# Optimization experiments

Measured on AMD Instinct MI355X. Metric: run time of the kernel, lower is better.

## Reference

```python
import jax, jax.numpy as jnp
import numpy as np

B, S, EPG = 1024, 64, 256          # graphs, nodes per graph, edges per graph
N, E = B * S, B * EPG              # 65536 nodes, 262144 edges
D, H = 128, 4                      # hidden dim, attention heads
DH = D // H
INIT_DIM, EDGE_DIM = 9, 3
N_EXTRA = 3                        # n_layers - 1
NEG_SLOPE = 0.2


def _gatv2(x, src, dst, edge_attr, Wl, Wr, bl, br, We, att, bias, heads, out_dim, concat):
    # PyG GATv2Conv with edge features: m = leaky_relu(xl[src]+xr[dst]+We@e),
    # alpha = segment_softmax(<m,att>, dst), out = scatter_add(alpha*xl[src], dst)
    n = x.shape[0]
    xl = (x @ Wl + bl).reshape(n, heads, out_dim)
    xr = (x @ Wr + br).reshape(n, heads, out_dim)
    ee = (edge_attr @ We).reshape(-1, heads, out_dim)
    m = jax.nn.leaky_relu(xl[src] + xr[dst] + ee, NEG_SLOPE)      # [E,H,O]
    logit = (m * att[None]).sum(-1)                               # [E,H]
    mx = jax.ops.segment_max(logit, dst, num_segments=n)
    ex = jnp.exp(logit - mx[dst])
    den = jax.ops.segment_sum(ex, dst, num_segments=n)
    alpha = ex / den[dst]                                         # segment softmax over in-edges
    out = jax.ops.segment_sum(xl[src] * alpha[:, :, None], dst, num_segments=n)
    out = out.reshape(n, heads * out_dim) if concat else out.mean(axis=1)
    return out + bias


def _forward(x, edge_index, edge_attr,
             g0_Wl, g0_Wr, g0_bl, g0_br, g0_We, g0_att, g0_bias,
             gWl, gWr, gbl, gbr, gWe, gatt, gbias,
             Wq, Wk, Wv, bq, bk, bv, Wo, bo):
    src, dst = edge_index[0], edge_index[1]
    h = _gatv2(x, src, dst, edge_attr, g0_Wl, g0_Wr, g0_bl, g0_br, g0_We, g0_att, g0_bias, 1, D, True)
    for i in range(N_EXTRA):
        h = (_gatv2(jax.nn.relu(h), src, dst, edge_attr,
                    gWl[i], gWr[i], gbl[i], gbr[i], gWe[i], gatt[i], gbias[i],
                    H, D, False) + h) / 2
    # to_dense_batch: equal-size graphs -> exact reshape, mask all True
    xd = h.reshape(B, S, D)
    q = (xd @ Wq + bq).reshape(B, S, H, DH)
    k = (xd @ Wk + bk).reshape(B, S, H, DH)
    v = (xd @ Wv + bv).reshape(B, S, H, DH)
    att = jax.nn.softmax(jnp.einsum('bqhd,bkhd->bhqk', q, k) / np.float32(np.sqrt(DH)), axis=-1)
    o = jnp.einsum('bhqk,bkhd->bqhd', att, v).reshape(B, S, D) @ Wo + bo
    return (h + o.reshape(N, D)) / 2


def setup_inputs():
    key = jax.random.key(0)
    ks = jax.random.split(key, 16)

    def gl(k, shape, fan):
        return jax.random.normal(k, shape, jnp.float32) / np.float32(np.sqrt(fan))

    x = jax.random.normal(ks[0], (N, INIT_DIM), jnp.float32)
    # random intra-graph edges: local indices in [0,S) offset per graph
    local = jax.random.randint(ks[1], (2, B, EPG), 0, S)
    edge_index = (local + (jnp.arange(B) * S)[None, :, None]).reshape(2, E)
    edge_attr = jax.random.normal(ks[2], (E, EDGE_DIM), jnp.float32)
    batch = jnp.repeat(jnp.arange(B), S)
    return dict(
        x=x, edge_index=edge_index, edge_attr=edge_attr, batch=batch,
        g0_Wl=gl(ks[3], (INIT_DIM, D), INIT_DIM), g0_Wr=gl(ks[4], (INIT_DIM, D), INIT_DIM),
        g0_bl=jnp.zeros((D,), jnp.float32), g0_br=jnp.zeros((D,), jnp.float32),
        g0_We=gl(ks[5], (EDGE_DIM, D), EDGE_DIM), g0_att=gl(ks[6], (1, D), D),
        g0_bias=jnp.zeros((D,), jnp.float32),
        gWl=gl(ks[7], (N_EXTRA, D, H * D), D), gWr=gl(ks[8], (N_EXTRA, D, H * D), D),
        gbl=jnp.zeros((N_EXTRA, H * D), jnp.float32), gbr=jnp.zeros((N_EXTRA, H * D), jnp.float32),
        gWe=gl(ks[9], (N_EXTRA, EDGE_DIM, H * D), EDGE_DIM), gatt=gl(ks[10], (N_EXTRA, H, D), D),
        gbias=jnp.zeros((N_EXTRA, D), jnp.float32),
        Wq=gl(ks[11], (D, D), D), Wk=gl(ks[12], (D, D), D), Wv=gl(ks[13], (D, D), D),
        bq=jnp.zeros((D,), jnp.float32), bk=jnp.zeros((D,), jnp.float32), bv=jnp.zeros((D,), jnp.float32),
        Wo=gl(ks[14], (D, D), D), bo=jnp.zeros((D,), jnp.float32),
    )


def reference(x, edge_index, edge_attr, batch,
              g0_Wl, g0_Wr, g0_bl, g0_br, g0_We, g0_att, g0_bias,
              gWl, gWr, gbl, gbr, gWe, gatt, gbias,
              Wq, Wk, Wv, bq, bk, bv, Wo, bo):
    # batch is implied by the equal-graph layout (reshape in _forward)
    return _forward(x, edge_index, edge_attr,
                    g0_Wl, g0_Wr, g0_bl, g0_br, g0_We, g0_att, g0_bias,
                    gWl, gWr, gbl, gbr, gWe, gatt, gbias,
                    Wq, Wk, Wv, bq, bk, bv, Wo, bo)
```

## Files before the change

kernel.cpp:

```cpp
#include <hip/hip_runtime.h>

constexpr int Bg  = 1024;
constexpr int Sg  = 64;
constexpr int EPG = 256;
constexpr int Nn  = Bg * Sg;
constexpr int Ne  = Bg * EPG;
constexpr int NH  = 4;
constexpr float NEG = 0.2f;

constexpr int CHUNK_G = 512;
constexpr int CHUNK_N = CHUNK_G * Sg;

typedef float  f32x4  __attribute__((ext_vector_type(4)));
typedef short  s16x8  __attribute__((ext_vector_type(8)));
typedef unsigned short u16x4 __attribute__((ext_vector_type(4)));

static __device__ __forceinline__ unsigned fenc(float f) {
    unsigned u = __float_as_uint(f);
    return (u & 0x80000000u) ? ~u : (u | 0x80000000u);
}
static __device__ __forceinline__ float fdec(unsigned k) {
    unsigned u = (k & 0x80000000u) ? (k ^ 0x80000000u) : ~k;
    return __uint_as_float(u);
}
static __device__ __forceinline__ unsigned short bf16rn(float x) {
    unsigned u = __float_as_uint(x);
    u += 0x7FFFu + ((u >> 16) & 1u);
    return (unsigned short)(u >> 16);
}
static __device__ __forceinline__ float bf16f(unsigned short h) {
    return __uint_as_float((unsigned)h << 16);
}
static __device__ __forceinline__ unsigned pack32(float x) {
    unsigned u  = __float_as_uint(x);
    unsigned hb = u & 0xffff0000u;
    float lof   = x - __uint_as_float(hb);
    return hb | (__float_as_uint(lof) >> 16);
}
static __device__ __forceinline__ float up_hi(unsigned u) {
    return __uint_as_float(u & 0xffff0000u);
}
static __device__ __forceinline__ float up_lo(unsigned u) {
    return __uint_as_float(u << 16);
}
#define DPP_ADD(x, ctrl) \
    ((x) + __int_as_float(__builtin_amdgcn_update_dpp( \
        0, __float_as_int(x), (ctrl), 0xF, 0xF, true)))

__global__ __launch_bounds__(256)
void wprep(const float* __restrict__ gWl, const float* __restrict__ gWr,
           const float* __restrict__ Wq, const float* __restrict__ Wk,
           const float* __restrict__ Wv, const float* __restrict__ Wo,
           unsigned short* __restrict__ whi, unsigned short* __restrict__ wlo) {
    int gid = blockIdx.x, t = threadIdx.x;
    const float* src;
    int n, k;
    size_t oidx;
    if (gid < 1536) {
        int s = gid >> 8;
        int e = ((gid & 255) << 8) + t;
        n = e & 511; k = e >> 9;
        src = (s & 1) ? (gWr + (s >> 1) * 65536) : (gWl + (s >> 1) * 65536);
        oidx = (size_t)s * 65536 + n * 128 + k;
        float v = src[k * 512 + n];
        unsigned short h = bf16rn(v);
        whi[oidx] = h;
        wlo[oidx] = bf16rn(v - bf16f(h));
    } else {
        int g2 = gid - 1536;
        int s = g2 >> 6;
        int e = ((g2 & 63) << 8) + t;
        n = e & 127; k = e >> 7;
        src = (s == 0) ? Wq : (s == 1) ? Wk : (s == 2) ? Wv : Wo;
        oidx = 393216 + (size_t)s * 16384 + n * 128 + k;
        float v = src[k * 128 + n];
        unsigned short h = bf16rn(v);
        whi[oidx] = h;
        wlo[oidx] = bf16rn(v - bf16f(h));
    }
}

__global__ __launch_bounds__(256)
void proj0(const float* __restrict__ x, const float* __restrict__ Wl,
           const float* __restrict__ Wr, const float* __restrict__ bl,
           const float* __restrict__ br, float* __restrict__ xl0,
           float* __restrict__ xr0) {
    int t = blockIdx.x * 256 + threadIdx.x;
    int n = t >> 7, j = t & 127;
    float xv[9];
#pragma unroll
    for (int k = 0; k < 9; ++k) xv[k] = x[n * 9 + k];
    float al = bl[j], ar = br[j];
#pragma unroll
    for (int k = 0; k < 9; ++k) {
        al = fmaf(xv[k], Wl[k * 128 + j], al);
        ar = fmaf(xv[k], Wr[k * 128 + j], ar);
    }
    xl0[t] = al;
    xr0[t] = ar;
}

template<bool RELU, int EPI>
__global__ __launch_bounds__(256, 2)
void gemm_mfma(const float* __restrict__ A, const unsigned short* __restrict__ wth,
               const unsigned short* __restrict__ wtl, const float* __restrict__ bias,
               const float* __restrict__ res, float* __restrict__ C, int NC) {
    __shared__ __align__(16) char smem[65536];
    constexpr int AH = 0, AL = 16384, BH = 32768, BL = 49152;

    const int t = threadIdx.x;
    const int r0 = blockIdx.y * 128, c0 = blockIdx.x * 128;
    const int wave = t >> 6, lane = t & 63;
    const int wm = wave >> 1, wn = wave & 1;
    const int lr = lane & 15, lg = lane >> 4;

    f32x4 acc[4][4] = {};

    int rowA[4], rowB[4];
#pragma unroll
    for (int i = 0; i < 4; ++i) {
        rowA[i] = wm * 64 + i * 16 + lr;
        rowB[i] = wn * 64 + i * 16 + lr;
    }

    for (int kc = 0; kc < 2; ++kc) {
#pragma unroll
        for (int i = 0; i < 8; ++i) {
            int f = t + i * 256;
            int row = f >> 4;
            int c4  = (f & 15) << 2;
            float4 v = *reinterpret_cast<const float4*>(
                &A[(size_t)(r0 + row) * 128 + kc * 64 + c4]);
            if (RELU) {
                v.x = fmaxf(v.x, 0.f); v.y = fmaxf(v.y, 0.f);
                v.z = fmaxf(v.z, 0.f); v.w = fmaxf(v.w, 0.f);
            }
            unsigned short h0 = bf16rn(v.x), h1 = bf16rn(v.y),
                           h2 = bf16rn(v.z), h3 = bf16rn(v.w);
            u16x4 hp = {h0, h1, h2, h3};
            u16x4 lp = {bf16rn(v.x - bf16f(h0)), bf16rn(v.y - bf16f(h1)),
                        bf16rn(v.z - bf16f(h2)), bf16rn(v.w - bf16f(h3))};
            int off = row * 128 + ((c4 * 2) ^ ((row & 7) << 4));
            *reinterpret_cast<u16x4*>(smem + AH + off) = hp;
            *reinterpret_cast<u16x4*>(smem + AL + off) = lp;
        }
#pragma unroll
        for (int i = 0; i < 4; ++i) {
            int f = t + i * 256;
            int row = f >> 3;
            int c8  = (f & 7) << 3;
            size_t gsrc = (size_t)(c0 + row) * 128 + kc * 64 + c8;
            s16x8 hv = *reinterpret_cast<const s16x8*>(&wth[gsrc]);
            s16x8 lv = *reinterpret_cast<const s16x8*>(&wtl[gsrc]);
            int off = row * 128 + ((c8 * 2) ^ ((row & 7) << 4));
            *reinterpret_cast<s16x8*>(smem + BH + off) = hv;
            *reinterpret_cast<s16x8*>(smem + BL + off) = lv;
        }
        __syncthreads();

#pragma unroll
        for (int ks = 0; ks < 2; ++ks) {
            const int kb = ks * 64 + lg * 16;
            s16x8 ah[4], al4[4];
#pragma unroll
            for (int mi = 0; mi < 4; ++mi) {
                int off = rowA[mi] * 128 + (kb ^ ((rowA[mi] & 7) << 4));
                ah[mi]  = *reinterpret_cast<const s16x8*>(smem + AH + off);
                al4[mi] = *reinterpret_cast<const s16x8*>(smem + AL + off);
            }
#pragma unroll
            for (int ni = 0; ni < 4; ++ni) {
                int off = rowB[ni] * 128 + (kb ^ ((rowB[ni] & 7) << 4));
                s16x8 bh = *reinterpret_cast<const s16x8*>(smem + BH + off);
                s16x8 bl = *reinterpret_cast<const s16x8*>(smem + BL + off);
#pragma unroll
                for (int mi = 0; mi < 4; ++mi) {
                    acc[mi][ni] = __builtin_amdgcn_mfma_f32_16x16x32_bf16(
                        ah[mi], bh, acc[mi][ni], 0, 0, 0);
                    acc[mi][ni] = __builtin_amdgcn_mfma_f32_16x16x32_bf16(
                        ah[mi], bl, acc[mi][ni], 0, 0, 0);
                    acc[mi][ni] = __builtin_amdgcn_mfma_f32_16x16x32_bf16(
                        al4[mi], bh, acc[mi][ni], 0, 0, 0);
                }
            }
        }
        __syncthreads();
    }

#pragma unroll
    for (int ni = 0; ni < 4; ++ni) {
        int c = c0 + wn * 64 + ni * 16 + lr;
        float bs = bias[c];
#pragma unroll
        for (int mi = 0; mi < 4; ++mi) {
#pragma unroll
            for (int j = 0; j < 4; ++j) {
                int r = r0 + wm * 64 + mi * 16 + lg * 4 + j;
                float ov = acc[mi][ni][j] + bs;
                if (EPI == 1) ov = (ov + res[(size_t)r * 128 + c]) * 0.5f;
                C[(size_t)r * NC + c] = ov;
            }
        }
    }
}

template<int HEADS, int EPI>
__global__ __launch_bounds__(512, 4)
void gat_edge(const float* __restrict__ xl, const float* __restrict__ xr,
              const int* __restrict__ ei, const float* __restrict__ ea,
              const float* __restrict__ We, const float* __restrict__ att,
              const float* __restrict__ bias, const float* __restrict__ hres,
              float* __restrict__ hout, int g0) {
    constexpr int WROW = HEADS * 128;
    __shared__ __align__(16) unsigned xli[64 * 128];
    __shared__ __align__(16) unsigned xri[64 * 128];
    __shared__ float eas[EPG * 4];
    __shared__ float logit[EPG];
    __shared__ int   se[EPG], de[EPG];
    __shared__ unsigned nmax[64];
    __shared__ float nden[64];

    const int g = g0 + blockIdx.x;
    const int t = threadIdx.x, lane = t & 63, wave = t >> 6;
    const int lr = lane & 15, lg = lane >> 4;
    const int wm = wave >> 2, wn = wave & 3;

    if (t < EPG) {
        se[t] = ei[g * EPG + t] - g * 64;
        de[t] = ei[Ne + g * EPG + t] - g * 64;
        eas[t * 4 + 0] = ea[(size_t)(g * EPG + t) * 3 + 0];
        eas[t * 4 + 1] = ea[(size_t)(g * EPG + t) * 3 + 1];
        eas[t * 4 + 2] = ea[(size_t)(g * EPG + t) * 3 + 2];
    }

    f32x4 acc[2][2] = {};
    float* P32 = reinterpret_cast<float*>(xri);

    for (int hh = 0; hh < HEADS; ++hh) {
        __syncthreads();
#pragma unroll
        for (int i = 0; i < 4; ++i) {
            int f  = t + i * 512;
            int r  = f >> 5;
            int c4 = (f & 31) << 2;
            size_t nl = (size_t)((g - g0) * 64 + r);
            float4 vl = *reinterpret_cast<const float4*>(&xl[nl * WROW + hh * 128 + c4]);
            float4 vr = *reinterpret_cast<const float4*>(&xr[nl * WROW + hh * 128 + c4]);
            uint4 pl = {pack32(vl.x), pack32(vl.y), pack32(vl.z), pack32(vl.w)};
            uint4 pr = {pack32(vr.x), pack32(vr.y), pack32(vr.z), pack32(vr.w)};
            *reinterpret_cast<uint4*>(&xli[r * 128 + c4]) = pl;
            *reinterpret_cast<uint4*>(&xri[r * 128 + c4]) = pr;
        }
        if (t < 64) { nmax[t] = 0u; nden[t] = 0.f; }
        __syncthreads();

        const float a1 = att[hh * 128 + 2 * lane];
        const float a2 = att[hh * 128 + 2 * lane + 1];
        float we1[3], we2[3];
#pragma unroll
        for (int k = 0; k < 3; ++k) {
            we1[k] = We[k * WROW + hh * 128 + 2 * lane];
            we2[k] = We[k * WROW + hh * 128 + 2 * lane + 1];
        }

        for (int e = wave; e < EPG; e += 8) {
            int s_ = se[e], d_ = de[e];
            float4 ev = *reinterpret_cast<const float4*>(&eas[e * 4]);
            uint2 ul = *reinterpret_cast<const uint2*>(&xli[s_ * 128 + 2 * lane]);
            uint2 ur = *reinterpret_cast<const uint2*>(&xri[d_ * 128 + 2 * lane]);
            float m1 = up_hi(ul.x) + up_lo(ul.x) + up_hi(ur.x) + up_lo(ur.x)
                       + ev.x * we1[0] + ev.y * we1[1] + ev.z * we1[2];
            float m2 = up_hi(ul.y) + up_lo(ul.y) + up_hi(ur.y) + up_lo(ur.y)
                       + ev.x * we2[0] + ev.y * we2[1] + ev.z * we2[2];
            m1 = m1 > 0.f ? m1 : NEG * m1;
            m2 = m2 > 0.f ? m2 : NEG * m2;
            float r = fmaf(m1, a1, m2 * a2);
            r = DPP_ADD(r, 0x111);
            r = DPP_ADD(r, 0x112);
            r = DPP_ADD(r, 0x114);
            r = DPP_ADD(r, 0x118);
            r = DPP_ADD(r, 0x142);
            r = DPP_ADD(r, 0x143);
            if (lane == 63) logit[e] = r;
        }
        __syncthreads();

        for (int i = t; i < 1088; i += 512)
            reinterpret_cast<float4*>(P32)[i] = float4{0.f, 0.f, 0.f, 0.f};
        if (t < EPG) atomicMax(&nmax[de[t]], fenc(logit[t]));
        __syncthreads();
        float ex = 0.f;
        if (t < EPG) {
            ex = __expf(logit[t] - fdec(nmax[de[t]]));
            atomicAdd(&nden[de[t]], ex);
        }
        __syncthreads();
        if (t < EPG) atomicAdd(&P32[de[t] * 68 + se[t]], ex / nden[de[t]]);
        __syncthreads();

#pragma unroll
        for (int ks = 0; ks < 2; ++ks) {
            s16x8 bh[2], bl[2];
#pragma unroll
            for (int nt = 0; nt < 2; ++nt) {
                int n = wn * 32 + nt * 16 + lr;
                unsigned uu[8];
#pragma unroll
                for (int j = 0; j < 8; ++j)
                    uu[j] = xli[(ks * 32 + lg * 8 + j) * 128 + n];
#pragma unroll
                for (int j = 0; j < 8; ++j) {
                    bh[nt][j] = (short)(uu[j] >> 16);
                    bl[nt][j] = (short)(uu[j] & 0xffffu);
                }
            }
#pragma unroll
            for (int mi = 0; mi < 2; ++mi) {
                const float* pr = &P32[(wm * 32 + mi * 16 + lr) * 68 + ks * 32 + lg * 8];
                float4 p0 = *reinterpret_cast<const float4*>(pr);
                float4 p1 = *reinterpret_cast<const float4*>(pr + 4);
                float pv[8] = {p0.x, p0.y, p0.z, p0.w, p1.x, p1.y, p1.z, p1.w};
                s16x8 pah, pal;
#pragma unroll
                for (int j = 0; j < 8; ++j) {
                    unsigned u = __float_as_uint(pv[j]);
                    unsigned hb = u & 0xffff0000u;
                    pah[j] = (short)(u >> 16);
                    pal[j] = (short)(__float_as_uint(pv[j] - __uint_as_float(hb)) >> 16);
                }
#pragma unroll
                for (int nt = 0; nt < 2; ++nt) {
                    acc[mi][nt] = __builtin_amdgcn_mfma_f32_16x16x32_bf16(
                        pah, bh[nt], acc[mi][nt], 0, 0, 0);
                    acc[mi][nt] = __builtin_amdgcn_mfma_f32_16x16x32_bf16(
                        pah, bl[nt], acc[mi][nt], 0, 0, 0);
                    acc[mi][nt] = __builtin_amdgcn_mfma_f32_16x16x32_bf16(
                        pal, bh[nt], acc[mi][nt], 0, 0, 0);
                }
            }
        }
    }

    constexpr float inv = 1.0f / (float)HEADS;
#pragma unroll
    for (int mi = 0; mi < 2; ++mi) {
#pragma unroll
        for (int nt = 0; nt < 2; ++nt) {
            int c_ = wn * 32 + nt * 16 + lr;
            float bs = bias[c_];
#pragma unroll
            for (int j = 0; j < 4; ++j) {
                int r_ = wm * 32 + mi * 16 + lg * 4 + j;
                size_t gi = (size_t)(g * 64 + r_) * 128 + c_;
                float v = acc[mi][nt][j] * inv + bs;
                if (EPI == 1) v = (v + hres[gi]) * 0.5f;
                hout[gi] = v;
            }
        }
    }
}

__global__ __launch_bounds__(256, 3)
void attn_k(const float* __restrict__ q, const float* __restrict__ k,
            const float* __restrict__ v, float* __restrict__ o) {
    __shared__ __align__(16) float qT[32 * 68];
    __shared__ __align__(16) float kT[32 * 68];
    __shared__ __align__(16) float vs[64 * 36];
    __shared__ __align__(16) float St[64 * 68];
    __shared__ float rden[64];

    const int g = blockIdx.x >> 2, hh = blockIdx.x & 3;
    const int t = threadIdx.x;

#pragma unroll
    for (int i = 0; i < 2; ++i) {
        int f = t + i * 256;
        int row = f >> 3;
        int c4  = (f & 7) << 2;
        size_t gi = (size_t)(g * 64 + row) * 128 + hh * 32 + c4;
        float4 qv = *reinterpret_cast<const float4*>(&q[gi]);
        float4 kv = *reinterpret_cast<const float4*>(&k[gi]);
        float4 vv = *reinterpret_cast<const float4*>(&v[gi]);
        qT[(c4 + 0) * 68 + row] = qv.x; qT[(c4 + 1) * 68 + row] = qv.y;
        qT[(c4 + 2) * 68 + row] = qv.z; qT[(c4 + 3) * 68 + row] = qv.w;
        kT[(c4 + 0) * 68 + row] = kv.x; kT[(c4 + 1) * 68 + row] = kv.y;
        kT[(c4 + 2) * 68 + row] = kv.z; kT[(c4 + 3) * 68 + row] = kv.w;
        *reinterpret_cast<float4*>(&vs[row * 36 + c4]) = vv;
    }
    __syncthreads();

    {
        const int rg = (t & 15) << 2, cg = (t >> 4) << 2;
        float acc[4][4] = {};
#pragma unroll 8
        for (int kk = 0; kk < 32; ++kk) {
            float4 qv = *reinterpret_cast<const float4*>(&qT[kk * 68 + rg]);
            float4 kv = *reinterpret_cast<const float4*>(&kT[kk * 68 + cg]);
            acc[0][0] = fmaf(qv.x, kv.x, acc[0][0]);
            acc[0][1] = fmaf(qv.x, kv.y, acc[0][1]);
            acc[0][2] = fmaf(qv.x, kv.z, acc[0][2]);
            acc[0][3] = fmaf(qv.x, kv.w, acc[0][3]);
            acc[1][0] = fmaf(qv.y, kv.x, acc[1][0]);
            acc[1][1] = fmaf(qv.y, kv.y, acc[1][1]);
            acc[1][2] = fmaf(qv.y, kv.z, acc[1][2]);
            acc[1][3] = fmaf(qv.y, kv.w, acc[1][3]);
            acc[2][0] = fmaf(qv.z, kv.x, acc[2][0]);
            acc[2][1] = fmaf(qv.z, kv.y, acc[2][1]);
            acc[2][2] = fmaf(qv.z, kv.z, acc[2][2]);
            acc[2][3] = fmaf(qv.z, kv.w, acc[2][3]);
            acc[3][0] = fmaf(qv.w, kv.x, acc[3][0]);
            acc[3][1] = fmaf(qv.w, kv.y, acc[3][1]);
            acc[3][2] = fmaf(qv.w, kv.z, acc[3][2]);
            acc[3][3] = fmaf(qv.w, kv.w, acc[3][3]);
        }
        constexpr float sc = 0.17677669529663687f;
#pragma unroll
        for (int j = 0; j < 4; ++j) {
            float4 sv;
            sv.x = acc[0][j] * sc; sv.y = acc[1][j] * sc;
            sv.z = acc[2][j] * sc; sv.w = acc[3][j] * sc;
            *reinterpret_cast<float4*>(&St[(cg + j) * 68 + rg]) = sv;
        }
    }
    __syncthreads();

    {
        const int r = t >> 2, q4 = t & 3;
        float mx = -3.4e38f;
#pragma unroll
        for (int i = 0; i < 16; ++i)
            mx = fmaxf(mx, St[(q4 * 16 + i) * 68 + r]);
        mx = fmaxf(mx, __shfl_xor(mx, 1, 64));
        mx = fmaxf(mx, __shfl_xor(mx, 2, 64));
        float sm = 0.f;
#pragma unroll
        for (int i = 0; i < 16; ++i) {
            int idx = (q4 * 16 + i) * 68 + r;
            float e = __expf(St[idx] - mx);
            St[idx] = e;
            sm += e;
        }
        sm += __shfl_xor(sm, 1, 64);
        sm += __shfl_xor(sm, 2, 64);
        if (q4 == 0) rden[r] = 1.f / sm;
    }
    __syncthreads();

    {
        const int rg = (t & 15) << 2, dg = (t >> 4) << 1;
        float a0 = 0.f, a1 = 0.f, a2 = 0.f, a3 = 0.f;
        float b0 = 0.f, b1 = 0.f, b2 = 0.f, b3 = 0.f;
#pragma unroll 8
        for (int kk = 0; kk < 64; ++kk) {
            float4 pv = *reinterpret_cast<const float4*>(&St[kk * 68 + rg]);
            float2 vv = *reinterpret_cast<const float2*>(&vs[kk * 36 + dg]);
            a0 = fmaf(pv.x, vv.x, a0); b0 = fmaf(pv.x, vv.y, b0);
            a1 = fmaf(pv.y, vv.x, a1); b1 = fmaf(pv.y, vv.y, b1);
            a2 = fmaf(pv.z, vv.x, a2); b2 = fmaf(pv.z, vv.y, b2);
            a3 = fmaf(pv.w, vv.x, a3); b3 = fmaf(pv.w, vv.y, b3);
        }
        float4 rd = *reinterpret_cast<const float4*>(&rden[rg]);
        float2 o0 = {a0 * rd.x, b0 * rd.x};
        float2 o1 = {a1 * rd.y, b1 * rd.y};
        float2 o2 = {a2 * rd.z, b2 * rd.z};
        float2 o3 = {a3 * rd.w, b3 * rd.w};
        size_t gb = (size_t)(g * 64 + rg) * 128 + hh * 32 + dg;
        *reinterpret_cast<float2*>(&o[gb])       = o0;
        *reinterpret_cast<float2*>(&o[gb + 128]) = o1;
        *reinterpret_cast<float2*>(&o[gb + 256]) = o2;
        *reinterpret_cast<float2*>(&o[gb + 384]) = o3;
    }
}

extern "C" void kernel_launch(void* const* d_in, const int* in_sizes, int n_in,
                              void* d_out, int out_size, void* d_ws, size_t ws_size,
                              hipStream_t stream) {
    const float* x     = (const float*)d_in[0];
    const int*   ei    = (const int*)d_in[1];
    const float* ea    = (const float*)d_in[2];
    const float* g0Wl  = (const float*)d_in[4];
    const float* g0Wr  = (const float*)d_in[5];
    const float* g0bl  = (const float*)d_in[6];
    const float* g0br  = (const float*)d_in[7];
    const float* g0We  = (const float*)d_in[8];
    const float* g0att = (const float*)d_in[9];
    const float* g0bias= (const float*)d_in[10];
    const float* gWl   = (const float*)d_in[11];
    const float* gWr   = (const float*)d_in[12];
    const float* gbl   = (const float*)d_in[13];
    const float* gbr   = (const float*)d_in[14];
    const float* gWe   = (const float*)d_in[15];
    const float* gatt  = (const float*)d_in[16];
    const float* gbias = (const float*)d_in[17];
    const float* Wq    = (const float*)d_in[18];
    const float* Wk    = (const float*)d_in[19];
    const float* Wv    = (const float*)d_in[20];
    const float* bq    = (const float*)d_in[21];
    const float* bk    = (const float*)d_in[22];
    const float* bv    = (const float*)d_in[23];
    const float* Wo    = (const float*)d_in[24];
    const float* bo    = (const float*)d_in[25];
    float* out = (float*)d_out;
    float* ws  = (float*)d_ws;

    float* h   = ws;
    float* xlb = ws + (size_t)Nn * 128;
    float* xrb = xlb + (size_t)CHUNK_N * 512;
    float* qb = xlb;
    float* kb = xlb + (size_t)Nn * 128;
    float* vb = xrb;
    float* ob = xrb + (size_t)Nn * 128;
    unsigned short* whi = (unsigned short*)(xrb + (size_t)CHUNK_N * 512);
    unsigned short* wlo = whi + 458752;

    wprep<<<1792, 256, 0, stream>>>(gWl, gWr, Wq, Wk, Wv, Wo, whi, wlo);

    proj0<<<Nn * 128 / 256, 256, 0, stream>>>(x, g0Wl, g0Wr, g0bl, g0br, xlb, xrb);
    gat_edge<1, 0><<<Bg, 512, 0, stream>>>(xlb, xrb, ei, ea, g0We, g0att,
                                           g0bias, nullptr, h, 0);

    for (int i = 0; i < 3; ++i) {
        for (int c = 0; c < 2; ++c) {
            const float* Ain = h + (size_t)c * CHUNK_N * 128;
            dim3 grid(512 / 128, CHUNK_N / 128);
            gemm_mfma<true, 0><<<grid, 256, 0, stream>>>(
                Ain, whi + (size_t)(2 * i) * 65536, wlo + (size_t)(2 * i) * 65536,
                gbl + i * 512, nullptr, xlb, 512);
            gemm_mfma<true, 0><<<grid, 256, 0, stream>>>(
                Ain, whi + (size_t)(2 * i + 1) * 65536, wlo + (size_t)(2 * i + 1) * 65536,
                gbr + i * 512, nullptr, xrb, 512);
            gat_edge<4, 1><<<CHUNK_G, 512, 0, stream>>>(
                xlb, xrb, ei, ea, gWe + (size_t)i * 3 * 512,
                gatt + (size_t)i * 4 * 128, gbias + i * 128, h, h, c * CHUNK_G);
        }
    }

    {
        dim3 grid(1, Nn / 128);
        gemm_mfma<false, 0><<<grid, 256, 0, stream>>>(h, whi + 393216, wlo + 393216,
                                                      bq, nullptr, qb, 128);
        gemm_mfma<false, 0><<<grid, 256, 0, stream>>>(h, whi + 409600, wlo + 409600,
                                                      bk, nullptr, kb, 128);
        gemm_mfma<false, 0><<<grid, 256, 0, stream>>>(h, whi + 425984, wlo + 425984,
                                                      bv, nullptr, vb, 128);
        attn_k<<<Bg * NH, 256, 0, stream>>>(qb, kb, vb, ob);
        gemm_mfma<false, 1><<<grid, 256, 0, stream>>>(ob, whi + 442368, wlo + 442368,
                                                      bo, h, out, 128);
    }
}
```

Before: 1.049 ms.

## Store intermediates in packed bf16 hi/lo format and swizzle GAT shared memory

Changes the storage format of xl/xr and h between kernels to packed 32-bit bf16 hi/lo pairs. Producers (proj0, gemm epilogue, gat_edge) write packed values and consumers split them directly, with no per-load fp32→bf16 conversion. ReLU on packed values becomes a sign-bit check. It also adds an XOR swizzle to the gat_edge shared-memory node tiles to reduce bank conflicts in the edge gather and MFMA B-operand reads. Memory traffic is unchanged (still 32 bits per element); the saving is in conversion ALU work and LDS conflicts. Precision changes slightly, because the final residual now uses the reconstructed hi+lo sum of h instead of the full fp32 value.

Measured after the change: 1.075 ms. 1.02x slower.

```diff
diff --git a/kernel.cpp b/kernel.cpp
--- a/kernel.cpp
+++ b/kernel.cpp
@@ -43,6 +43,13 @@
 static __device__ __forceinline__ float up_lo(unsigned u) {
     return __uint_as_float(u << 16);
 }
+static __device__ __forceinline__ float unpk(unsigned u) {
+    return up_hi(u) + up_lo(u);
+}
+static __device__ __forceinline__ unsigned relu_pk(unsigned u) {
+    return ((int)u < 0) ? 0u : u;
+}
+#define SWZ(r) (((((r) >> 3) & 1) << 4) | ((((r) >> 3) & 2) << 1))
 #define DPP_ADD(x, ctrl) \
     ((x) + __int_as_float(__builtin_amdgcn_update_dpp( \
         0, __float_as_int(x), (ctrl), 0xF, 0xF, true)))
@@ -83,8 +90,8 @@
 __global__ __launch_bounds__(256)
 void proj0(const float* __restrict__ x, const float* __restrict__ Wl,
            const float* __restrict__ Wr, const float* __restrict__ bl,
-           const float* __restrict__ br, float* __restrict__ xl0,
-           float* __restrict__ xr0) {
+           const float* __restrict__ br, unsigned* __restrict__ xl0,
+           unsigned* __restrict__ xr0) {
     int t = blockIdx.x * 256 + threadIdx.x;
     int n = t >> 7, j = t & 127;
     float xv[9];
@@ -96,15 +103,15 @@
         al = fmaf(xv[k], Wl[k * 128 + j], al);
         ar = fmaf(xv[k], Wr[k * 128 + j], ar);
     }
-    xl0[t] = al;
-    xr0[t] = ar;
-}
-
-template<bool RELU, int EPI>
+    xl0[t] = pack32(al);
+    xr0[t] = pack32(ar);
+}
+
+template<int IN_MODE, int OUT_MODE>
 __global__ __launch_bounds__(256, 2)
-void gemm_mfma(const float* __restrict__ A, const unsigned short* __restrict__ wth,
+void gemm_mfma(const void* __restrict__ Av, const unsigned short* __restrict__ wth,
                const unsigned short* __restrict__ wtl, const float* __restrict__ bias,
-               const float* __restrict__ res, float* __restrict__ C, int NC) {
+               const unsigned* __restrict__ hres, void* __restrict__ Cv, int NC) {
     __shared__ __align__(16) char smem[65536];
     constexpr int AH = 0, AL = 16384, BH = 32768, BL = 49152;
 
@@ -129,17 +136,27 @@
             int f = t + i * 256;
             int row = f >> 4;
             int c4  = (f & 15) << 2;
-            float4 v = *reinterpret_cast<const float4*>(
-                &A[(size_t)(r0 + row) * 128 + kc * 64 + c4]);
-            if (RELU) {
-                v.x = fmaxf(v.x, 0.f); v.y = fmaxf(v.y, 0.f);
-                v.z = fmaxf(v.z, 0.f); v.w = fmaxf(v.w, 0.f);
-            }
-            unsigned short h0 = bf16rn(v.x), h1 = bf16rn(v.y),
-                           h2 = bf16rn(v.z), h3 = bf16rn(v.w);
-            u16x4 hp = {h0, h1, h2, h3};
-            u16x4 lp = {bf16rn(v.x - bf16f(h0)), bf16rn(v.y - bf16f(h1)),
-                        bf16rn(v.z - bf16f(h2)), bf16rn(v.w - bf16f(h3))};
+            u16x4 hp, lp;
+            if (IN_MODE == 0) {
+                float4 v = *reinterpret_cast<const float4*>(
+                    &((const float*)Av)[(size_t)(r0 + row) * 128 + kc * 64 + c4]);
+                unsigned short h0 = bf16rn(v.x), h1 = bf16rn(v.y),
+                               h2 = bf16rn(v.z), h3 = bf16rn(v.w);
+                hp = u16x4{h0, h1, h2, h3};
+                lp = u16x4{bf16rn(v.x - bf16f(h0)), bf16rn(v.y - bf16f(h1)),
+                           bf16rn(v.z - bf16f(h2)), bf16rn(v.w - bf16f(h3))};
+            } else {
+                uint4 u = *reinterpret_cast<const uint4*>(
+                    &((const unsigned*)Av)[(size_t)(r0 + row) * 128 + kc * 64 + c4]);
+                if (IN_MODE == 2) {
+                    u.x = relu_pk(u.x); u.y = relu_pk(u.y);
+                    u.z = relu_pk(u.z); u.w = relu_pk(u.w);
+                }
+                hp = u16x4{(unsigned short)(u.x >> 16), (unsigned short)(u.y >> 16),
+                           (unsigned short)(u.z >> 16), (unsigned short)(u.w >> 16)};
+                lp = u16x4{(unsigned short)(u.x & 0xffffu), (unsigned short)(u.y & 0xffffu),
+                           (unsigned short)(u.z & 0xffffu), (unsigned short)(u.w & 0xffffu)};
+            }
             int off = row * 128 + ((c4 * 2) ^ ((row & 7) << 4));
             *reinterpret_cast<u16x4*>(smem + AH + off) = hp;
             *reinterpret_cast<u16x4*>(smem + AL + off) = lp;
@@ -197,8 +214,14 @@
             for (int j = 0; j < 4; ++j) {
                 int r = r0 + wm * 64 + mi * 16 + lg * 4 + j;
                 float ov = acc[mi][ni][j] + bs;
-                if (EPI == 1) ov = (ov + res[(size_t)r * 128 + c]) * 0.5f;
-                C[(size_t)r * NC + c] = ov;
+                if (OUT_MODE == 0) {
+                    ((unsigned*)Cv)[(size_t)r * NC + c] = pack32(ov);
+                } else if (OUT_MODE == 1) {
+                    ((float*)Cv)[(size_t)r * NC + c] = ov;
+                } else {
+                    ov = (ov + unpk(hres[(size_t)r * 128 + c])) * 0.5f;
+                    ((float*)Cv)[(size_t)r * NC + c] = ov;
+                }
             }
         }
     }
@@ -206,11 +229,11 @@
 
 template<int HEADS, int EPI>
 __global__ __launch_bounds__(512, 4)
-void gat_edge(const float* __restrict__ xl, const float* __restrict__ xr,
+void gat_edge(const unsigned* __restrict__ xl, const unsigned* __restrict__ xr,
               const int* __restrict__ ei, const float* __restrict__ ea,
               const float* __restrict__ We, const float* __restrict__ att,
-              const float* __restrict__ bias, const float* __restrict__ hres,
-              float* __restrict__ hout, int g0) {
+              const float* __restrict__ bias, const unsigned* __restrict__ hres,
+              unsigned* __restrict__ hout, int g0) {
     constexpr int WROW = HEADS * 128;
     __shared__ __align__(16) unsigned xli[64 * 128];
     __shared__ __align__(16) unsigned xri[64 * 128];
@@ -224,6 +247,7 @@
     const int t = threadIdx.x, lane = t & 63, wave = t >> 6;
     const int lr = lane & 15, lg = lane >> 4;
     const int wm = wave >> 2, wn = wave & 3;
+    const int swzB = ((lg & 1) << 4) | ((lg & 2) << 1);
 
     if (t < EPG) {
         se[t] = ei[g * EPG + t] - g * 64;
@@ -244,12 +268,11 @@
             int r  = f >> 5;
             int c4 = (f & 31) << 2;
             size_t nl = (size_t)((g - g0) * 64 + r);
-            float4 vl = *reinterpret_cast<const float4*>(&xl[nl * WROW + hh * 128 + c4]);
-            float4 vr = *reinterpret_cast<const float4*>(&xr[nl * WROW + hh * 128 + c4]);
-            uint4 pl = {pack32(vl.x), pack32(vl.y), pack32(vl.z), pack32(vl.w)};
-            uint4 pr = {pack32(vr.x), pack32(vr.y), pack32(vr.z), pack32(vr.w)};
-            *reinterpret_cast<uint4*>(&xli[r * 128 + c4]) = pl;
-            *reinterpret_cast<uint4*>(&xri[r * 128 + c4]) = pr;
+            uint4 pl = *reinterpret_cast<const uint4*>(&xl[nl * WROW + hh * 128 + c4]);
+            uint4 pr = *reinterpret_cast<const uint4*>(&xr[nl * WROW + hh * 128 + c4]);
+            int cs = c4 ^ SWZ(r);
+            *reinterpret_cast<uint4*>(&xli[r * 128 + cs]) = pl;
+            *reinterpret_cast<uint4*>(&xri[r * 128 + cs]) = pr;
         }
         if (t < 64) { nmax[t] = 0u; nden[t] = 0.f; }
         __syncthreads();
@@ -266,11 +289,13 @@
         for (int e = wave; e < EPG; e += 8) {
             int s_ = se[e], d_ = de[e];
             float4 ev = *reinterpret_cast<const float4*>(&eas[e * 4]);
-            uint2 ul = *reinterpret_cast<const uint2*>(&xli[s_ * 128 + 2 * lane]);
-            uint2 ur = *reinterpret_cast<const uint2*>(&xri[d_ * 128 + 2 * lane]);
-            float m1 = up_hi(ul.x) + up_lo(ul.x) + up_hi(ur.x) + up_lo(ur.x)
+            uint2 ul = *reinterpret_cast<const uint2*>(
+                &xli[s_ * 128 + ((2 * lane) ^ SWZ(s_))]);
+            uint2 ur = *reinterpret_cast<const uint2*>(
+                &xri[d_ * 128 + ((2 * lane) ^ SWZ(d_))]);
+            float m1 = unpk(ul.x) + unpk(ur.x)
                        + ev.x * we1[0] + ev.y * we1[1] + ev.z * we1[2];
-            float m2 = up_hi(ul.y) + up_lo(ul.y) + up_hi(ur.y) + up_lo(ur.y)
+            float m2 = unpk(ul.y) + unpk(ur.y)
                        + ev.x * we2[0] + ev.y * we2[1] + ev.z * we2[2];
             m1 = m1 > 0.f ? m1 : NEG * m1;
             m2 = m2 > 0.f ? m2 : NEG * m2;
@@ -303,7 +328,7 @@
             s16x8 bh[2], bl[2];
 #pragma unroll
             for (int nt = 0; nt < 2; ++nt) {
-                int n = wn * 32 + nt * 16 + lr;
+                int n = (wn * 32 + nt * 16 + lr) ^ swzB;
                 unsigned uu[8];
 #pragma unroll
                 for (int j = 0; j < 8; ++j)
@@ -353,8 +378,8 @@
                 int r_ = wm * 32 + mi * 16 + lg * 4 + j;
                 size_t gi = (size_t)(g * 64 + r_) * 128 + c_;
                 float v = acc[mi][nt][j] * inv + bs;
-                if (EPI == 1) v = (v + hres[gi]) * 0.5f;
-                hout[gi] = v;
+                if (EPI == 1) v = (v + unpk(hres[gi])) * 0.5f;
+                hout[gi] = pack32(v);
             }
         }
     }
@@ -501,15 +526,14 @@
     const float* Wo    = (const float*)d_in[24];
     const float* bo    = (const float*)d_in[25];
     float* out = (float*)d_out;
-    float* ws  = (float*)d_ws;
-
-    float* h   = ws;
-    float* xlb = ws + (size_t)Nn * 128;
-    float* xrb = xlb + (size_t)CHUNK_N * 512;
-    float* qb = xlb;
-    float* kb = xlb + (size_t)Nn * 128;
-    float* vb = xrb;
-    float* ob = xrb + (size_t)Nn * 128;
+
+    unsigned* h   = (unsigned*)d_ws;
+    unsigned* xlb = h + (size_t)Nn * 128;
+    unsigned* xrb = xlb + (size_t)CHUNK_N * 512;
+    float* qb = (float*)xlb;
+    float* kb = (float*)(xlb + (size_t)Nn * 128);
+    float* vb = (float*)xrb;
+    float* ob = (float*)(xrb + (size_t)Nn * 128);
     unsigned short* whi = (unsigned short*)(xrb + (size_t)CHUNK_N * 512);
     unsigned short* wlo = whi + 458752;
 
@@ -521,12 +545,12 @@
 
     for (int i = 0; i < 3; ++i) {
         for (int c = 0; c < 2; ++c) {
-            const float* Ain = h + (size_t)c * CHUNK_N * 128;
+            const unsigned* Ain = h + (size_t)c * CHUNK_N * 128;
             dim3 grid(512 / 128, CHUNK_N / 128);
-            gemm_mfma<true, 0><<<grid, 256, 0, stream>>>(
+            gemm_mfma<2, 0><<<grid, 256, 0, stream>>>(
                 Ain, whi + (size_t)(2 * i) * 65536, wlo + (size_t)(2 * i) * 65536,
                 gbl + i * 512, nullptr, xlb, 512);
-            gemm_mfma<true, 0><<<grid, 256, 0, stream>>>(
+            gemm_mfma<2, 0><<<grid, 256, 0, stream>>>(
                 Ain, whi + (size_t)(2 * i + 1) * 65536, wlo + (size_t)(2 * i + 1) * 65536,
                 gbr + i * 512, nullptr, xrb, 512);
             gat_edge<4, 1><<<CHUNK_G, 512, 0, stream>>>(
@@ -537,14 +561,14 @@
 
     {
         dim3 grid(1, Nn / 128);
-        gemm_mfma<false, 0><<<grid, 256, 0, stream>>>(h, whi + 393216, wlo + 393216,
-                                                      bq, nullptr, qb, 128);
-        gemm_mfma<false, 0><<<grid, 256, 0, stream>>>(h, whi + 409600, wlo + 409600,
-                                                      bk, nullptr, kb, 128);
-        gemm_mfma<false, 0><<<grid, 256, 0, stream>>>(h, whi + 425984, wlo + 425984,
-                                                      bv, nullptr, vb, 128);
+        gemm_mfma<1, 1><<<grid, 256, 0, stream>>>(h, whi + 393216, wlo + 393216,
+                                                  bq, nullptr, qb, 128);
+        gemm_mfma<1, 1><<<grid, 256, 0, stream>>>(h, whi + 409600, wlo + 409600,
+                                                  bk, nullptr, kb, 128);
+        gemm_mfma<1, 1><<<grid, 256, 0, stream>>>(h, whi + 425984, wlo + 425984,
+                                                  bv, nullptr, vb, 128);
         attn_k<<<Bg * NH, 256, 0, stream>>>(qb, kb, vb, ob);
-        gemm_mfma<false, 1><<<grid, 256, 0, stream>>>(ob, whi + 442368, wlo + 442368,
-                                                      bo, h, out, 128);
-    }
-}
+        gemm_mfma<0, 2><<<grid, 256, 0, stream>>>(ob, whi + 442368, wlo + 442368,
+                                                  bo, h, out, 128);
+    }
+}
```
